# Performance work log

Measured on AMD Instinct MI355X. Metric: run time of the kernel, lower is better.

## Reference

```python
import jax, jax.numpy as jnp
import numpy as np
from jax.scipy.linalg import solve_triangular

NUM_EMBEDDINGS = 512
EMBEDDING_DIM = 64
SPARSITY = 5
COMMITMENT_COST = 0.25


def batch_omp(data, dictionary, max_nonzero):
    """Batch OMP. data: (M, B), dictionary: (M, N). Returns coeffs (N, B)."""
    M, B = data.shape
    Dt = dictionary.T                       # (N, M)
    G = Dt @ dictionary                     # (N, N) Gram matrix
    h_bar = (Dt @ data).T                   # (B, N)
    h = h_bar
    x = jnp.zeros_like(h_bar)               # (B, N)
    L = jnp.ones((B, 1, 1), data.dtype)     # growing Cholesky factor
    mask = jnp.zeros(h_bar.shape, dtype=bool)
    I = None                                # selected atom indices (B, k)
    bidx = jnp.arange(B)
    for k in range(1, max_nonzero + 1):     # small fixed unroll (5 iters)
        index = jnp.argmax(jnp.abs(h * (~mask)), axis=1)   # (B,)
        mask = mask.at[bidx, index].set(True)
        if k > 1:
            # G[I_b, index_b] for each batch element -> (B, k-1, 1)
            G_stack = G[I, index[:, None]][..., None]
            w = solve_triangular(L, G_stack, lower=True)   # (B, k-1, 1)
            wT = jnp.swapaxes(w, 1, 2)                     # (B, 1, k-1)
            w_corner = jnp.sqrt(jnp.clip(1.0 - jnp.sum(wT ** 2, axis=2, keepdims=True), 0.0))
            top = jnp.concatenate([L, jnp.zeros((B, k - 1, 1), L.dtype)], axis=2)
            bot = jnp.concatenate([wT, w_corner], axis=2)
            L = jnp.concatenate([top, bot], axis=1)        # (B, k, k)
            I = jnp.concatenate([I, index[:, None]], axis=1)
        else:
            I = index[:, None]
        h_stack = jnp.take_along_axis(h_bar, I, axis=1)[..., None]  # (B, k, 1)
        y = solve_triangular(L, h_stack, lower=True)
        x_stack = solve_triangular(jnp.swapaxes(L, 1, 2), y, lower=False)  # (B, k, 1)
        x = x.at[bidx[:, None], I].set(x_stack[..., 0])
        beta = jnp.einsum('bk,bkn->bn', x_stack[..., 0], G[I])  # (B, N)
        h = h_bar - beta
    return x.T                              # (N, B)


def setup_inputs() -> dict:
    key = jax.random.key(0)
    k1, k2 = jax.random.split(key)
    z_e = jax.random.normal(k1, (32, EMBEDDING_DIM, 32, 32), dtype=jnp.float32)
    D = jax.random.normal(k2, (EMBEDDING_DIM, NUM_EMBEDDINGS), dtype=jnp.float32)
    D = D / jnp.linalg.norm(D, axis=0)      # column-normalized atoms (as _normalize_dictionary)
    return {"z_e": z_e, "dictionary": D}


def reference(z_e, dictionary):
    # permute BCHW -> BHWC, then flat view to (embedding_dim, -1) row-major (as torch .view)
    z_perm = jnp.transpose(z_e, (0, 2, 3, 1))          # (B, H, W, C)
    input_shape = z_perm.shape
    ze_flat = z_perm.reshape(EMBEDDING_DIM, -1)        # (M, Btokens)
    coefficients = batch_omp(ze_flat, dictionary, SPARSITY)  # (N, Btokens)
    z_dl = (dictionary @ coefficients).reshape(input_shape)
    e_latent_loss = jnp.mean((jax.lax.stop_gradient(z_dl) - z_perm) ** 2)
    dl_latent_loss = jnp.mean((z_dl - jax.lax.stop_gradient(z_perm)) ** 2)
    loss = COMMITMENT_COST * e_latent_loss + dl_latent_loss
    z_out = z_perm + jax.lax.stop_gradient(z_dl - z_perm)   # straight-through
    return (jnp.transpose(z_out, (0, 3, 1, 2)), loss, coefficients)
```

## Files before the change

### kernel.cpp

```cpp
#include <hip/hip_runtime.h>

#define B_TOTAL 32768
#define NATOM   512
#define MDIM    64
#define KS      5

__global__ void k_perm(const float* __restrict__ ze, float* __restrict__ dT) {
    const int n   = blockIdx.x >> 4;
    const int hw0 = (blockIdx.x & 15) * 64;
    const int t   = threadIdx.x;
    __shared__ float lds[64][65];
#pragma unroll
    for (int r = 0; r < 16; ++r) {
        int id = r * 256 + t;
        int c = id >> 6, i = id & 63;
        lds[c][i] = ze[n * 65536 + c * 1024 + hw0 + i];
    }
    __syncthreads();
#pragma unroll
    for (int r = 0; r < 16; ++r) {
        int id = r * 256 + t;
        int c = id & 63, j = id >> 6;
        int hw = hw0 + j;
        int h = hw >> 5, w = hw & 31;
        int m = (n << 1) | (h >> 4);
        int b = ((h & 15) << 11) | (w << 6) | c;
        dT[m * 32768 + b] = lds[c][j];
    }
}

__global__ void k_gram(const float* __restrict__ D, float* __restrict__ G,
                       float* __restrict__ acc) {
    const int i = blockIdx.x;
    const int t = threadIdx.x;
    __shared__ float col[MDIM];
    if (t < MDIM) col[t] = D[t * NATOM + i];
    __syncthreads();
    for (int j = t; j < NATOM; j += 256) {
        float s = 0.f;
#pragma unroll
        for (int m = 0; m < MDIM; ++m) s = fmaf(col[m], D[m * NATOM + j], s);
        G[i * NATOM + j] = s;
    }
    if (i == 0 && t == 0) *acc = 0.f;
}

__launch_bounds__(256, 2)
__global__ void k_omp(const float* __restrict__ data, const float* __restrict__ D,
                      const float* __restrict__ G, int* __restrict__ idx_out,
                      float* __restrict__ val_out) {
    const int t    = threadIdx.x;
    const int lane = t & 63;
    const int wv   = t >> 6;
    const int b0   = blockIdx.x * 32;

    __shared__ __align__(16) float data_s[32][68];
    __shared__ __align__(16) float stage[4][2048];
    __shared__ int   idx_s[KS][32];
    __shared__ float val_s[KS][32];

#pragma unroll
    for (int r = 0; r < 8; ++r) {
        int id = r * 256 + t;
        int m = id >> 5, bb = id & 31;
        data_s[bb][m] = data[m * B_TOTAL + b0 + bb];
    }
    __syncthreads();

    const float4* __restrict__ D4 = (const float4*)D;
    const float4* __restrict__ G4 = (const float4*)G;

    float4 acc[8][2];
#pragma unroll
    for (int bb = 0; bb < 8; ++bb) {
        acc[bb][0] = make_float4(0.f, 0.f, 0.f, 0.f);
        acc[bb][1] = make_float4(0.f, 0.f, 0.f, 0.f);
    }
    const int bwbase = wv * 8;

#pragma unroll 4
    for (int c = 0; c < 16; ++c) {
        float4 df[4][2];
#pragma unroll
        for (int mm = 0; mm < 4; ++mm) {
            df[mm][0] = D4[(c * 4 + mm) * 128 + lane];
            df[mm][1] = D4[(c * 4 + mm) * 128 + 64 + lane];
        }
#pragma unroll
        for (int bb = 0; bb < 8; ++bb) {
            const float4 dv = *(const float4*)&data_s[bwbase + bb][c * 4];
            const float dm[4] = {dv.x, dv.y, dv.z, dv.w};
#pragma unroll
            for (int mm = 0; mm < 4; ++mm) {
                acc[bb][0].x = fmaf(df[mm][0].x, dm[mm], acc[bb][0].x);
                acc[bb][0].y = fmaf(df[mm][0].y, dm[mm], acc[bb][0].y);
                acc[bb][0].z = fmaf(df[mm][0].z, dm[mm], acc[bb][0].z);
                acc[bb][0].w = fmaf(df[mm][0].w, dm[mm], acc[bb][0].w);
                acc[bb][1].x = fmaf(df[mm][1].x, dm[mm], acc[bb][1].x);
                acc[bb][1].y = fmaf(df[mm][1].y, dm[mm], acc[bb][1].y);
                acc[bb][1].z = fmaf(df[mm][1].z, dm[mm], acc[bb][1].z);
                acc[bb][1].w = fmaf(df[mm][1].w, dm[mm], acc[bb][1].w);
            }
        }
    }

    const int g = lane >> 3;
    const int p = lane & 7;
    float hb[64];
#pragma unroll
    for (int r = 0; r < 2; ++r) {
        __syncthreads();
#pragma unroll
        for (int q2 = 0; q2 < 4; ++q2) {
            int bb = r * 4 + q2;
            *(float4*)&stage[wv][q2 * 512 + 4 * lane]       = acc[bb][0];
            *(float4*)&stage[wv][q2 * 512 + 256 + 4 * lane] = acc[bb][1];
        }
        __syncthreads();
        if ((g >> 2) == r) {
#pragma unroll
            for (int q = 0; q < 16; ++q) {
                const float4 v =
                    *(const float4*)&stage[wv][(g & 3) * 512 + 32 * q + 4 * p];
                hb[4 * q + 0] = v.x;
                hb[4 * q + 1] = v.y;
                hb[4 * q + 2] = v.z;
                hb[4 * q + 3] = v.w;
            }
        }
    }

    float key[64];
#pragma unroll
    for (int e = 0; e < 64; ++e) key[e] = fabsf(hb[e]);

    unsigned msk0 = 0u, msk1 = 0u;
    int   I[KS];
    float xs[KS];
    float gsel[KS];
    float Lm[15];

#pragma unroll
    for (int k = 0; k < KS; ++k) {
        float bv = key[0]; int be = 0; float bhb = hb[0];
#pragma unroll
        for (int e = 1; e < 64; ++e) {
            bool gt = key[e] > bv;
            bv  = gt ? key[e] : bv;
            be  = gt ? e      : be;
            bhb = gt ? hb[e]  : bhb;
        }
        int bn = 32 * (be >> 2) + 4 * p + (be & 3);
#pragma unroll
        for (int off = 1; off < 8; off <<= 1) {
            float ov  = __shfl_xor(bv, off);
            int   on  = __shfl_xor(bn, off);
            float ohb = __shfl_xor(bhb, off);
            bool take = (ov > bv) || (ov == bv && on < bn);
            bv = take ? ov : bv; bn = take ? on : bn; bhb = take ? ohb : bhb;
        }
        const int nsel = bn;
        I[k]    = nsel;
        gsel[k] = bhb;

        {
            int own  = (nsel >> 2) & 7;
            int esel = ((nsel >> 5) << 2) | (nsel & 3);
            if (p == own) {
                if (esel < 32) msk0 |= 1u << esel;
                else           msk1 |= 1u << (esel - 32);
            }
        }

        if (k > 0) {
            float gk[KS - 1], w[KS - 1];
#pragma unroll
            for (int ti = 0; ti < KS - 1; ++ti)
                if (ti < k) gk[ti] = G[I[ti] * NATOM + nsel];
#pragma unroll
            for (int r = 0; r < KS - 1; ++r) {
                if (r < k) {
                    float s = gk[r];
#pragma unroll
                    for (int cc = 0; cc < KS - 1; ++cc)
                        if (cc < r) s -= Lm[r * (r + 1) / 2 + cc] * w[cc];
                    w[r] = s / Lm[r * (r + 1) / 2 + r];
                }
            }
            float s2 = 0.f;
#pragma unroll
            for (int r = 0; r < KS - 1; ++r) if (r < k) s2 += w[r] * w[r];
            float wc = sqrtf(fmaxf(0.f, 1.f - s2));
#pragma unroll
            for (int cc = 0; cc < KS - 1; ++cc)
                if (cc < k) Lm[k * (k + 1) / 2 + cc] = w[cc];
            Lm[k * (k + 1) / 2 + k] = wc;
        } else {
            Lm[0] = 1.f;
        }

        float y[KS];
#pragma unroll
        for (int r = 0; r <= k; ++r) {
            float s = gsel[r];
#pragma unroll
            for (int cc = 0; cc < r; ++cc) s -= Lm[r * (r + 1) / 2 + cc] * y[cc];
            y[r] = s / Lm[r * (r + 1) / 2 + r];
        }
#pragma unroll
        for (int r = k; r >= 0; --r) {
            float s = y[r];
#pragma unroll
            for (int cc = r + 1; cc <= k; ++cc) s -= Lm[cc * (cc + 1) / 2 + r] * xs[cc];
            xs[r] = s / Lm[r * (r + 1) / 2 + r];
        }

        if (k < KS - 1) {
#pragma unroll
            for (int q = 0; q < 16; ++q) {
                float bx = 0.f, by = 0.f, bz = 0.f, bw = 0.f;
#pragma unroll
                for (int ti = 0; ti < KS - 1; ++ti) {
                    if (ti <= k) {
                        const float4 gc = G4[I[ti] * 128 + 8 * q + p];
                        bx = fmaf(xs[ti], gc.x, bx);
                        by = fmaf(xs[ti], gc.y, by);
                        bz = fmaf(xs[ti], gc.z, bz);
                        bw = fmaf(xs[ti], gc.w, bw);
                    }
                }
                {
                    float d0 = hb[4 * q + 0] - bx;
                    float d1 = hb[4 * q + 1] - by;
                    float d2 = hb[4 * q + 2] - bz;
                    float d3 = hb[4 * q + 3] - bw;
                    const int e0 = 4 * q;
                    bool m0 = (e0 + 0 < 32) ? ((msk0 >> (e0 + 0)) & 1u) : ((msk1 >> (e0 - 32)) & 1u);
                    bool m1 = (e0 + 1 < 32) ? ((msk0 >> (e0 + 1)) & 1u) : ((msk1 >> (e0 + 1 - 32)) & 1u);
                    bool m2 = (e0 + 2 < 32) ? ((msk0 >> (e0 + 2)) & 1u) : ((msk1 >> (e0 + 2 - 32)) & 1u);
                    bool m3 = (e0 + 3 < 32) ? ((msk0 >> (e0 + 3)) & 1u) : ((msk1 >> (e0 + 3 - 32)) & 1u);
                    key[e0 + 0] = m0 ? -1.f : fabsf(d0);
                    key[e0 + 1] = m1 ? -1.f : fabsf(d1);
                    key[e0 + 2] = m2 ? -1.f : fabsf(d2);
                    key[e0 + 3] = m3 ? -1.f : fabsf(d3);
                }
            }
        }
    }

    if (p == 0) {
#pragma unroll
        for (int k = 0; k < KS; ++k) {
            idx_s[k][wv * 8 + g] = I[k];
            val_s[k][wv * 8 + g] = xs[k];
        }
    }
    __syncthreads();
    if (t < KS * 32) {
        int k = t >> 5, bb = t & 31;
        idx_out[k * B_TOTAL + b0 + bb] = idx_s[k][bb];
        val_out[k * B_TOTAL + b0 + bb] = val_s[k][bb];
    }
}

__global__ void k_coeff(const int* __restrict__ idx, const float* __restrict__ val,
                        float* __restrict__ coeff) {
    const int bblk = blockIdx.x >> 3;
    const int jc   = blockIdx.x & 7;
    const int b    = bblk * 256 + threadIdx.x;
    int   I[KS]; float V[KS];
#pragma unroll
    for (int k = 0; k < KS; ++k) {
        I[k] = idx[k * B_TOTAL + b];
        V[k] = val[k * B_TOTAL + b];
    }
    const int j0 = jc * 64;
#pragma unroll 4
    for (int j = j0; j < j0 + 64; ++j) {
        float w = 0.f;
#pragma unroll
        for (int k = 0; k < KS; ++k) w = (I[k] == j) ? V[k] : w;
        coeff[j * B_TOTAL + b] = w;
    }
}

__global__ void k_recon(const float* __restrict__ dataT, const float* __restrict__ D,
                        const int* __restrict__ idx, const float* __restrict__ val,
                        float* __restrict__ zout, float* __restrict__ acc) {
    const int n   = blockIdx.x >> 4;
    const int hw0 = (blockIdx.x & 15) * 64;
    const int t   = threadIdx.x;
    __shared__ float lds[64][65];
    float sq = 0.f;
#pragma unroll
    for (int r = 0; r < 16; ++r) {
        int id = r * 256 + t;
        int c = id & 63, j = id >> 6;
        int f = n * 65536 + (hw0 + j) * 64 + c;
        int b = f & 32767;
        int m = f >> 15;
        float zdl = 0.f;
#pragma unroll
        for (int k = 0; k < KS; ++k) {
            int   a = idx[k * B_TOTAL + b];
            float v = val[k * B_TOTAL + b];
            zdl = fmaf(v, D[m * NATOM + a], zdl);
        }
        float zp   = dataT[f];
        float diff = zdl - zp;
        lds[c][j] = zp + diff;
        sq = fmaf(diff, diff, sq);
    }
    __syncthreads();
#pragma unroll
    for (int r = 0; r < 16; ++r) {
        int id = r * 256 + t;
        int cc = id >> 6, i = id & 63;
        zout[n * 65536 + cc * 1024 + hw0 + i] = lds[cc][i];
    }
#pragma unroll
    for (int off = 32; off > 0; off >>= 1) sq += __shfl_xor(sq, off);
    __shared__ float red[4];
    if ((t & 63) == 0) red[t >> 6] = sq;
    __syncthreads();
    if (t == 0) atomicAdd(acc, red[0] + red[1] + red[2] + red[3]);
}

__global__ void k_loss(const float* __restrict__ acc, float* __restrict__ out_loss) {
    if (threadIdx.x == 0 && blockIdx.x == 0)
        *out_loss = 1.25f * (*acc / 2097152.f);
}

extern "C" void kernel_launch(void* const* d_in, const int* in_sizes, int n_in,
                              void* d_out, int out_size, void* d_ws, size_t ws_size,
                              hipStream_t stream) {
    const float* ze = (const float*)d_in[0];
    const float* D  = (const float*)d_in[1];

    float* G     = (float*)d_ws;
    int*   idxp  = (int*)  ((char*)d_ws + (size_t)262144 * 4);
    float* valp  = (float*)((char*)d_ws + (size_t)(262144 + 163840) * 4);
    float* accp  = (float*)((char*)d_ws + (size_t)(262144 + 2 * 163840) * 4);
    float* dataT = (float*)((char*)d_ws + (size_t)(262144 + 2 * 163840 + 64) * 4);

    float* zout  = (float*)d_out;
    float* lossp = zout + 2097152;
    float* coeff = zout + 2097153;

    k_perm <<<512, 256, 0, stream>>>(ze, dataT);
    k_gram <<<512, 256, 0, stream>>>(D, G, accp);
    k_omp  <<<1024, 256, 0, stream>>>(dataT, D, G, idxp, valp);
    k_coeff<<<1024, 256, 0, stream>>>(idxp, valp, coeff);
    k_recon<<<512, 256, 0, stream>>>(dataT, D, idxp, valp, zout, accp);
    k_loss <<<1, 64, 0, stream>>>(accp, lossp);
}
```

Baseline: 186.9 us.

## Merge independent launches, keep residual h in registers with incremental update

Fuses the permute and Gram kernels into one launch, and the coefficient scatter and reconstruction kernels into another, cutting launch count from six to four. Inside the OMP kernel, the separate hb and key register arrays are replaced by a single residual array h. It is updated incrementally with the change in coefficients, and the argmax is split into four independent chains to shorten the dependency chain. The staging buffer is halved, and the selected h_bar value is rebuilt from the residual plus the Gram correction. This lowers register pressure and launch overhead, at the cost of possible small floating-point drift in the incremental residual.

```diff
diff --git a/kernel.cpp b/kernel.cpp
--- a/kernel.cpp
+++ b/kernel.cpp
@@ -5,44 +5,44 @@
 #define MDIM    64
 #define KS      5
 
-__global__ void k_perm(const float* __restrict__ ze, float* __restrict__ dT) {
-    const int n   = blockIdx.x >> 4;
-    const int hw0 = (blockIdx.x & 15) * 64;
-    const int t   = threadIdx.x;
+__global__ void k_prep(const float* __restrict__ ze, float* __restrict__ dT,
+                       const float* __restrict__ D, float* __restrict__ G,
+                       float* __restrict__ acc) {
     __shared__ float lds[64][65];
-#pragma unroll
-    for (int r = 0; r < 16; ++r) {
-        int id = r * 256 + t;
-        int c = id >> 6, i = id & 63;
-        lds[c][i] = ze[n * 65536 + c * 1024 + hw0 + i];
-    }
-    __syncthreads();
-#pragma unroll
-    for (int r = 0; r < 16; ++r) {
-        int id = r * 256 + t;
-        int c = id & 63, j = id >> 6;
-        int hw = hw0 + j;
-        int h = hw >> 5, w = hw & 31;
-        int m = (n << 1) | (h >> 4);
-        int b = ((h & 15) << 11) | (w << 6) | c;
-        dT[m * 32768 + b] = lds[c][j];
-    }
-}
-
-__global__ void k_gram(const float* __restrict__ D, float* __restrict__ G,
-                       float* __restrict__ acc) {
-    const int i = blockIdx.x;
     const int t = threadIdx.x;
-    __shared__ float col[MDIM];
-    if (t < MDIM) col[t] = D[t * NATOM + i];
-    __syncthreads();
-    for (int j = t; j < NATOM; j += 256) {
-        float s = 0.f;
-#pragma unroll
-        for (int m = 0; m < MDIM; ++m) s = fmaf(col[m], D[m * NATOM + j], s);
-        G[i * NATOM + j] = s;
-    }
-    if (i == 0 && t == 0) *acc = 0.f;
+    if (blockIdx.x < 512) {
+        const int n   = blockIdx.x >> 4;
+        const int hw0 = (blockIdx.x & 15) * 64;
+#pragma unroll
+        for (int r = 0; r < 16; ++r) {
+            int id = r * 256 + t;
+            int c = id >> 6, i = id & 63;
+            lds[c][i] = ze[n * 65536 + c * 1024 + hw0 + i];
+        }
+        __syncthreads();
+#pragma unroll
+        for (int r = 0; r < 16; ++r) {
+            int id = r * 256 + t;
+            int c = id & 63, j = id >> 6;
+            int hw = hw0 + j;
+            int h = hw >> 5, w = hw & 31;
+            int m = (n << 1) | (h >> 4);
+            int b = ((h & 15) << 11) | (w << 6) | c;
+            dT[m * 32768 + b] = lds[c][j];
+        }
+    } else {
+        const int i = blockIdx.x - 512;
+        float* col = &lds[0][0];
+        if (t < MDIM) col[t] = D[t * NATOM + i];
+        __syncthreads();
+        for (int j = t; j < NATOM; j += 256) {
+            float s = 0.f;
+#pragma unroll
+            for (int m = 0; m < MDIM; ++m) s = fmaf(col[m], D[m * NATOM + j], s);
+            G[i * NATOM + j] = s;
+        }
+        if (i == 0 && t == 0) *acc = 0.f;
+    }
 }
 
 __launch_bounds__(256, 2)
@@ -55,7 +55,7 @@
     const int b0   = blockIdx.x * 32;
 
     __shared__ __align__(16) float data_s[32][68];
-    __shared__ __align__(16) float stage[4][2048];
+    __shared__ __align__(16) float stage[4][1024];
     __shared__ int   idx_s[KS][32];
     __shared__ float val_s[KS][32];
 
@@ -106,33 +106,29 @@
 
     const int g = lane >> 3;
     const int p = lane & 7;
-    float hb[64];
-#pragma unroll
-    for (int r = 0; r < 2; ++r) {
-        __syncthreads();
-#pragma unroll
-        for (int q2 = 0; q2 < 4; ++q2) {
-            int bb = r * 4 + q2;
+    float h[64];
+#pragma unroll
+    for (int r = 0; r < 4; ++r) {
+        __syncthreads();
+#pragma unroll
+        for (int q2 = 0; q2 < 2; ++q2) {
+            int bb = r * 2 + q2;
             *(float4*)&stage[wv][q2 * 512 + 4 * lane]       = acc[bb][0];
             *(float4*)&stage[wv][q2 * 512 + 256 + 4 * lane] = acc[bb][1];
         }
         __syncthreads();
-        if ((g >> 2) == r) {
+        if ((g >> 1) == r) {
 #pragma unroll
             for (int q = 0; q < 16; ++q) {
                 const float4 v =
-                    *(const float4*)&stage[wv][(g & 3) * 512 + 32 * q + 4 * p];
-                hb[4 * q + 0] = v.x;
-                hb[4 * q + 1] = v.y;
-                hb[4 * q + 2] = v.z;
-                hb[4 * q + 3] = v.w;
-            }
-        }
-    }
-
-    float key[64];
-#pragma unroll
-    for (int e = 0; e < 64; ++e) key[e] = fabsf(hb[e]);
+                    *(const float4*)&stage[wv][(g & 1) * 512 + 32 * q + 4 * p];
+                h[4 * q + 0] = v.x;
+                h[4 * q + 1] = v.y;
+                h[4 * q + 2] = v.z;
+                h[4 * q + 3] = v.w;
+            }
+        }
+    }
 
     unsigned msk0 = 0u, msk1 = 0u;
     int   I[KS];
@@ -142,26 +138,38 @@
 
 #pragma unroll
     for (int k = 0; k < KS; ++k) {
-        float bv = key[0]; int be = 0; float bhb = hb[0];
-#pragma unroll
-        for (int e = 1; e < 64; ++e) {
-            bool gt = key[e] > bv;
-            bv  = gt ? key[e] : bv;
-            be  = gt ? e      : be;
-            bhb = gt ? hb[e]  : bhb;
+        float cv[4]; int ce[4]; float ch[4];
+#pragma unroll
+        for (int c4 = 0; c4 < 4; ++c4) {
+            cv[c4] = fabsf(h[16 * c4]); ce[c4] = 16 * c4; ch[c4] = h[16 * c4];
+#pragma unroll
+            for (int e = 16 * c4 + 1; e < 16 * c4 + 16; ++e) {
+                float a = fabsf(h[e]);
+                bool gt = a > cv[c4];
+                cv[c4] = gt ? a    : cv[c4];
+                ce[c4] = gt ? e    : ce[c4];
+                ch[c4] = gt ? h[e] : ch[c4];
+            }
+        }
+        float bv = cv[0]; int be = ce[0]; float bh = ch[0];
+#pragma unroll
+        for (int c4 = 1; c4 < 4; ++c4) {
+            bool gt = cv[c4] > bv;
+            bv = gt ? cv[c4] : bv;
+            be = gt ? ce[c4] : be;
+            bh = gt ? ch[c4] : bh;
         }
         int bn = 32 * (be >> 2) + 4 * p + (be & 3);
 #pragma unroll
         for (int off = 1; off < 8; off <<= 1) {
-            float ov  = __shfl_xor(bv, off);
-            int   on  = __shfl_xor(bn, off);
-            float ohb = __shfl_xor(bhb, off);
+            float ov = __shfl_xor(bv, off);
+            int   on = __shfl_xor(bn, off);
+            float oh = __shfl_xor(bh, off);
             bool take = (ov > bv) || (ov == bv && on < bn);
-            bv = take ? ov : bv; bn = take ? on : bn; bhb = take ? ohb : bhb;
+            bv = take ? ov : bv; bn = take ? on : bn; bh = take ? oh : bh;
         }
         const int nsel = bn;
-        I[k]    = nsel;
-        gsel[k] = bhb;
+        I[k] = nsel;
 
         {
             int own  = (nsel >> 2) & 7;
@@ -177,6 +185,11 @@
 #pragma unroll
             for (int ti = 0; ti < KS - 1; ++ti)
                 if (ti < k) gk[ti] = G[I[ti] * NATOM + nsel];
+            float hb_sel = bh;
+#pragma unroll
+            for (int ti = 0; ti < KS - 1; ++ti)
+                if (ti < k) hb_sel = fmaf(xs[ti], gk[ti], hb_sel);
+            gsel[k] = hb_sel;
 #pragma unroll
             for (int r = 0; r < KS - 1; ++r) {
                 if (r < k) {
@@ -196,6 +209,7 @@
                 if (cc < k) Lm[k * (k + 1) / 2 + cc] = w[cc];
             Lm[k * (k + 1) / 2 + k] = wc;
         } else {
+            gsel[0] = bh;
             Lm[0] = 1.f;
         }
 
@@ -207,6 +221,9 @@
             for (int cc = 0; cc < r; ++cc) s -= Lm[r * (r + 1) / 2 + cc] * y[cc];
             y[r] = s / Lm[r * (r + 1) / 2 + r];
         }
+        float dx[KS];
+#pragma unroll
+        for (int ti = 0; ti < KS; ++ti) dx[ti] = (ti < k) ? xs[ti] : 0.f;
 #pragma unroll
         for (int r = k; r >= 0; --r) {
             float s = y[r];
@@ -214,6 +231,8 @@
             for (int cc = r + 1; cc <= k; ++cc) s -= Lm[cc * (cc + 1) / 2 + r] * xs[cc];
             xs[r] = s / Lm[r * (r + 1) / 2 + r];
         }
+#pragma unroll
+        for (int ti = 0; ti < KS; ++ti) if (ti <= k) dx[ti] = xs[ti] - dx[ti];
 
         if (k < KS - 1) {
 #pragma unroll
@@ -223,26 +242,26 @@
                 for (int ti = 0; ti < KS - 1; ++ti) {
                     if (ti <= k) {
                         const float4 gc = G4[I[ti] * 128 + 8 * q + p];
-                        bx = fmaf(xs[ti], gc.x, bx);
-                        by = fmaf(xs[ti], gc.y, by);
-                        bz = fmaf(xs[ti], gc.z, bz);
-                        bw = fmaf(xs[ti], gc.w, bw);
+                        bx = fmaf(dx[ti], gc.x, bx);
+                        by = fmaf(dx[ti], gc.y, by);
+                        bz = fmaf(dx[ti], gc.z, bz);
+                        bw = fmaf(dx[ti], gc.w, bw);
                     }
                 }
                 {
-                    float d0 = hb[4 * q + 0] - bx;
-                    float d1 = hb[4 * q + 1] - by;
-                    float d2 = hb[4 * q + 2] - bz;
-                    float d3 = hb[4 * q + 3] - bw;
+                    float d0 = h[4 * q + 0] - bx;
+                    float d1 = h[4 * q + 1] - by;
+                    float d2 = h[4 * q + 2] - bz;
+                    float d3 = h[4 * q + 3] - bw;
                     const int e0 = 4 * q;
                     bool m0 = (e0 + 0 < 32) ? ((msk0 >> (e0 + 0)) & 1u) : ((msk1 >> (e0 - 32)) & 1u);
                     bool m1 = (e0 + 1 < 32) ? ((msk0 >> (e0 + 1)) & 1u) : ((msk1 >> (e0 + 1 - 32)) & 1u);
                     bool m2 = (e0 + 2 < 32) ? ((msk0 >> (e0 + 2)) & 1u) : ((msk1 >> (e0 + 2 - 32)) & 1u);
                     bool m3 = (e0 + 3 < 32) ? ((msk0 >> (e0 + 3)) & 1u) : ((msk1 >> (e0 + 3 - 32)) & 1u);
-                    key[e0 + 0] = m0 ? -1.f : fabsf(d0);
-                    key[e0 + 1] = m1 ? -1.f : fabsf(d1);
-                    key[e0 + 2] = m2 ? -1.f : fabsf(d2);
-                    key[e0 + 3] = m3 ? -1.f : fabsf(d3);
+                    h[e0 + 0] = m0 ? 0.f : d0;
+                    h[e0 + 1] = m1 ? 0.f : d1;
+                    h[e0 + 2] = m2 ? 0.f : d2;
+                    h[e0 + 3] = m3 ? 0.f : d3;
                 }
             }
         }
@@ -263,67 +282,68 @@
     }
 }
 
-__global__ void k_coeff(const int* __restrict__ idx, const float* __restrict__ val,
-                        float* __restrict__ coeff) {
-    const int bblk = blockIdx.x >> 3;
-    const int jc   = blockIdx.x & 7;
-    const int b    = bblk * 256 + threadIdx.x;
-    int   I[KS]; float V[KS];
-#pragma unroll
-    for (int k = 0; k < KS; ++k) {
-        I[k] = idx[k * B_TOTAL + b];
-        V[k] = val[k * B_TOTAL + b];
-    }
-    const int j0 = jc * 64;
+__global__ void k_post(const int* __restrict__ idx, const float* __restrict__ val,
+                       float* __restrict__ coeff, const float* __restrict__ dataT,
+                       const float* __restrict__ D, float* __restrict__ zout,
+                       float* __restrict__ acc) {
+    __shared__ float lds[64][65];
+    const int t = threadIdx.x;
+    if (blockIdx.x < 1024) {
+        const int bblk = blockIdx.x >> 3;
+        const int jc   = blockIdx.x & 7;
+        const int b    = bblk * 256 + t;
+        int   I[KS]; float V[KS];
+#pragma unroll
+        for (int k = 0; k < KS; ++k) {
+            I[k] = idx[k * B_TOTAL + b];
+            V[k] = val[k * B_TOTAL + b];
+        }
+        const int j0 = jc * 64;
 #pragma unroll 4
-    for (int j = j0; j < j0 + 64; ++j) {
-        float w = 0.f;
-#pragma unroll
-        for (int k = 0; k < KS; ++k) w = (I[k] == j) ? V[k] : w;
-        coeff[j * B_TOTAL + b] = w;
-    }
-}
-
-__global__ void k_recon(const float* __restrict__ dataT, const float* __restrict__ D,
-                        const int* __restrict__ idx, const float* __restrict__ val,
-                        float* __restrict__ zout, float* __restrict__ acc) {
-    const int n   = blockIdx.x >> 4;
-    const int hw0 = (blockIdx.x & 15) * 64;
-    const int t   = threadIdx.x;
-    __shared__ float lds[64][65];
-    float sq = 0.f;
-#pragma unroll
-    for (int r = 0; r < 16; ++r) {
-        int id = r * 256 + t;
-        int c = id & 63, j = id >> 6;
-        int f = n * 65536 + (hw0 + j) * 64 + c;
-        int b = f & 32767;
-        int m = f >> 15;
-        float zdl = 0.f;
-#pragma unroll
-        for (int k = 0; k < KS; ++k) {
-            int   a = idx[k * B_TOTAL + b];
-            float v = val[k * B_TOTAL + b];
-            zdl = fmaf(v, D[m * NATOM + a], zdl);
-        }
-        float zp   = dataT[f];
-        float diff = zdl - zp;
-        lds[c][j] = zp + diff;
-        sq = fmaf(diff, diff, sq);
-    }
-    __syncthreads();
-#pragma unroll
-    for (int r = 0; r < 16; ++r) {
-        int id = r * 256 + t;
-        int cc = id >> 6, i = id & 63;
-        zout[n * 65536 + cc * 1024 + hw0 + i] = lds[cc][i];
-    }
-#pragma unroll
-    for (int off = 32; off > 0; off >>= 1) sq += __shfl_xor(sq, off);
-    __shared__ float red[4];
-    if ((t & 63) == 0) red[t >> 6] = sq;
-    __syncthreads();
-    if (t == 0) atomicAdd(acc, red[0] + red[1] + red[2] + red[3]);
+        for (int j = j0; j < j0 + 64; ++j) {
+            float w = 0.f;
+#pragma unroll
+            for (int k = 0; k < KS; ++k) w = (I[k] == j) ? V[k] : w;
+            coeff[j * B_TOTAL + b] = w;
+        }
+    } else {
+        const int blk = blockIdx.x - 1024;
+        const int n   = blk >> 4;
+        const int hw0 = (blk & 15) * 64;
+        float sq = 0.f;
+#pragma unroll
+        for (int r = 0; r < 16; ++r) {
+            int id = r * 256 + t;
+            int c = id & 63, j = id >> 6;
+            int f = n * 65536 + (hw0 + j) * 64 + c;
+            int b = f & 32767;
+            int m = f >> 15;
+            float zdl = 0.f;
+#pragma unroll
+            for (int k = 0; k < KS; ++k) {
+                int   a = idx[k * B_TOTAL + b];
+                float v = val[k * B_TOTAL + b];
+                zdl = fmaf(v, D[m * NATOM + a], zdl);
+            }
+            float zp   = dataT[f];
+            float diff = zdl - zp;
+            lds[c][j] = zp + diff;
+            sq = fmaf(diff, diff, sq);
+        }
+        __syncthreads();
+#pragma unroll
+        for (int r = 0; r < 16; ++r) {
+            int id = r * 256 + t;
+            int cc = id >> 6, i = id & 63;
+            zout[n * 65536 + cc * 1024 + hw0 + i] = lds[cc][i];
+        }
+#pragma unroll
+        for (int off = 32; off > 0; off >>= 1) sq += __shfl_xor(sq, off);
+        __shared__ float red[4];
+        if ((t & 63) == 0) red[t >> 6] = sq;
+        __syncthreads();
+        if (t == 0) atomicAdd(acc, red[0] + red[1] + red[2] + red[3]);
+    }
 }
 
 __global__ void k_loss(const float* __restrict__ acc, float* __restrict__ out_loss) {
@@ -347,10 +367,8 @@
     float* lossp = zout + 2097152;
     float* coeff = zout + 2097153;
 
-    k_perm <<<512, 256, 0, stream>>>(ze, dataT);
-    k_gram <<<512, 256, 0, stream>>>(D, G, accp);
-    k_omp  <<<1024, 256, 0, stream>>>(dataT, D, G, idxp, valp);
-    k_coeff<<<1024, 256, 0, stream>>>(idxp, valp, coeff);
-    k_recon<<<512, 256, 0, stream>>>(dataT, D, idxp, valp, zout, accp);
-    k_loss <<<1, 64, 0, stream>>>(accp, lossp);
-}
+    k_prep<<<1024, 256, 0, stream>>>(ze, dataT, D, G, accp);
+    k_omp <<<1024, 256, 0, stream>>>(dataT, D, G, idxp, valp);
+    k_post<<<1536, 256, 0, stream>>>(idxp, valp, coeff, dataT, D, zout, accp);
+    k_loss<<<1, 64, 0, stream>>>(accp, lossp);
+}
```

Result: faster. 182.0 us (-2.6%).

## Merge independent kernels and shrink OMP blocks to single wavefronts

Applied to the files above, without the earlier changes.

Permute and Gram computation now share one launch, split by block index, and coefficient scatter and reconstruction share another, which cuts the kernel count from six to four. The OMP kernel drops from four wavefronts over 32 tokens to one wavefront over 8 tokens. This removes block-wide barriers and the LDS staging of results, and it lets the scheduler fit more small blocks per CU. In exchange, each block now loads the dictionary on its own, four times as often as before, and the larger number of small blocks adds scheduling overhead.

```diff
diff --git a/kernel.cpp b/kernel.cpp
--- a/kernel.cpp
+++ b/kernel.cpp
@@ -5,64 +5,60 @@
 #define MDIM    64
 #define KS      5
 
-__global__ void k_perm(const float* __restrict__ ze, float* __restrict__ dT) {
-    const int n   = blockIdx.x >> 4;
-    const int hw0 = (blockIdx.x & 15) * 64;
-    const int t   = threadIdx.x;
+__global__ void k_prep(const float* __restrict__ ze, float* __restrict__ dT,
+                       const float* __restrict__ D, float* __restrict__ G,
+                       float* __restrict__ acc) {
     __shared__ float lds[64][65];
-#pragma unroll
-    for (int r = 0; r < 16; ++r) {
-        int id = r * 256 + t;
-        int c = id >> 6, i = id & 63;
-        lds[c][i] = ze[n * 65536 + c * 1024 + hw0 + i];
-    }
-    __syncthreads();
-#pragma unroll
-    for (int r = 0; r < 16; ++r) {
-        int id = r * 256 + t;
-        int c = id & 63, j = id >> 6;
-        int hw = hw0 + j;
-        int h = hw >> 5, w = hw & 31;
-        int m = (n << 1) | (h >> 4);
-        int b = ((h & 15) << 11) | (w << 6) | c;
-        dT[m * 32768 + b] = lds[c][j];
-    }
-}
-
-__global__ void k_gram(const float* __restrict__ D, float* __restrict__ G,
-                       float* __restrict__ acc) {
-    const int i = blockIdx.x;
     const int t = threadIdx.x;
-    __shared__ float col[MDIM];
-    if (t < MDIM) col[t] = D[t * NATOM + i];
-    __syncthreads();
-    for (int j = t; j < NATOM; j += 256) {
-        float s = 0.f;
-#pragma unroll
-        for (int m = 0; m < MDIM; ++m) s = fmaf(col[m], D[m * NATOM + j], s);
-        G[i * NATOM + j] = s;
-    }
-    if (i == 0 && t == 0) *acc = 0.f;
-}
-
-__launch_bounds__(256, 2)
+    if (blockIdx.x < 512) {
+        const int n   = blockIdx.x >> 4;
+        const int hw0 = (blockIdx.x & 15) * 64;
+#pragma unroll
+        for (int r = 0; r < 16; ++r) {
+            int id = r * 256 + t;
+            int c = id >> 6, i = id & 63;
+            lds[c][i] = ze[n * 65536 + c * 1024 + hw0 + i];
+        }
+        __syncthreads();
+#pragma unroll
+        for (int r = 0; r < 16; ++r) {
+            int id = r * 256 + t;
+            int c = id & 63, j = id >> 6;
+            int hw = hw0 + j;
+            int h = hw >> 5, w = hw & 31;
+            int m = (n << 1) | (h >> 4);
+            int b = ((h & 15) << 11) | (w << 6) | c;
+            dT[m * 32768 + b] = lds[c][j];
+        }
+    } else {
+        const int i = blockIdx.x - 512;
+        float* col = &lds[0][0];
+        if (t < MDIM) col[t] = D[t * NATOM + i];
+        __syncthreads();
+        for (int j = t; j < NATOM; j += 256) {
+            float s = 0.f;
+#pragma unroll
+            for (int m = 0; m < MDIM; ++m) s = fmaf(col[m], D[m * NATOM + j], s);
+            G[i * NATOM + j] = s;
+        }
+        if (i == 0 && t == 0) *acc = 0.f;
+    }
+}
+
+__launch_bounds__(64, 4)
 __global__ void k_omp(const float* __restrict__ data, const float* __restrict__ D,
                       const float* __restrict__ G, int* __restrict__ idx_out,
                       float* __restrict__ val_out) {
-    const int t    = threadIdx.x;
-    const int lane = t & 63;
-    const int wv   = t >> 6;
-    const int b0   = blockIdx.x * 32;
-
-    __shared__ __align__(16) float data_s[32][68];
-    __shared__ __align__(16) float stage[4][2048];
-    __shared__ int   idx_s[KS][32];
-    __shared__ float val_s[KS][32];
+    const int lane = threadIdx.x;
+    const int b0   = blockIdx.x * 8;
+
+    __shared__ __align__(16) float data_s[8][68];
+    __shared__ __align__(16) float stage[2048];
 
 #pragma unroll
     for (int r = 0; r < 8; ++r) {
-        int id = r * 256 + t;
-        int m = id >> 5, bb = id & 31;
+        int id = r * 64 + lane;
+        int m = id >> 3, bb = id & 7;
         data_s[bb][m] = data[m * B_TOTAL + b0 + bb];
     }
     __syncthreads();
@@ -76,7 +72,6 @@
         acc[bb][0] = make_float4(0.f, 0.f, 0.f, 0.f);
         acc[bb][1] = make_float4(0.f, 0.f, 0.f, 0.f);
     }
-    const int bwbase = wv * 8;
 
 #pragma unroll 4
     for (int c = 0; c < 16; ++c) {
@@ -88,7 +83,7 @@
         }
 #pragma unroll
         for (int bb = 0; bb < 8; ++bb) {
-            const float4 dv = *(const float4*)&data_s[bwbase + bb][c * 4];
+            const float4 dv = *(const float4*)&data_s[bb][c * 4];
             const float dm[4] = {dv.x, dv.y, dv.z, dv.w};
 #pragma unroll
             for (int mm = 0; mm < 4; ++mm) {
@@ -113,15 +108,15 @@
 #pragma unroll
         for (int q2 = 0; q2 < 4; ++q2) {
             int bb = r * 4 + q2;
-            *(float4*)&stage[wv][q2 * 512 + 4 * lane]       = acc[bb][0];
-            *(float4*)&stage[wv][q2 * 512 + 256 + 4 * lane] = acc[bb][1];
+            *(float4*)&stage[q2 * 512 + 4 * lane]       = acc[bb][0];
+            *(float4*)&stage[q2 * 512 + 256 + 4 * lane] = acc[bb][1];
         }
         __syncthreads();
         if ((g >> 2) == r) {
 #pragma unroll
             for (int q = 0; q < 16; ++q) {
                 const float4 v =
-                    *(const float4*)&stage[wv][(g & 3) * 512 + 32 * q + 4 * p];
+                    *(const float4*)&stage[(g & 3) * 512 + 32 * q + 4 * p];
                 hb[4 * q + 0] = v.x;
                 hb[4 * q + 1] = v.y;
                 hb[4 * q + 2] = v.z;
@@ -251,79 +246,74 @@
     if (p == 0) {
 #pragma unroll
         for (int k = 0; k < KS; ++k) {
-            idx_s[k][wv * 8 + g] = I[k];
-            val_s[k][wv * 8 + g] = xs[k];
-        }
-    }
-    __syncthreads();
-    if (t < KS * 32) {
-        int k = t >> 5, bb = t & 31;
-        idx_out[k * B_TOTAL + b0 + bb] = idx_s[k][bb];
-        val_out[k * B_TOTAL + b0 + bb] = val_s[k][bb];
-    }
-}
-
-__global__ void k_coeff(const int* __restrict__ idx, const float* __restrict__ val,
-                        float* __restrict__ coeff) {
-    const int bblk = blockIdx.x >> 3;
-    const int jc   = blockIdx.x & 7;
-    const int b    = bblk * 256 + threadIdx.x;
-    int   I[KS]; float V[KS];
-#pragma unroll
-    for (int k = 0; k < KS; ++k) {
-        I[k] = idx[k * B_TOTAL + b];
-        V[k] = val[k * B_TOTAL + b];
-    }
-    const int j0 = jc * 64;
+            idx_out[k * B_TOTAL + b0 + g] = I[k];
+            val_out[k * B_TOTAL + b0 + g] = xs[k];
+        }
+    }
+}
+
+__global__ void k_post(const int* __restrict__ idx, const float* __restrict__ val,
+                       float* __restrict__ coeff, const float* __restrict__ dataT,
+                       const float* __restrict__ D, float* __restrict__ zout,
+                       float* __restrict__ acc) {
+    __shared__ float lds[64][65];
+    const int t = threadIdx.x;
+    if (blockIdx.x < 1024) {
+        const int bblk = blockIdx.x >> 3;
+        const int jc   = blockIdx.x & 7;
+        const int b    = bblk * 256 + t;
+        int   I[KS]; float V[KS];
+#pragma unroll
+        for (int k = 0; k < KS; ++k) {
+            I[k] = idx[k * B_TOTAL + b];
+            V[k] = val[k * B_TOTAL + b];
+        }
+        const int j0 = jc * 64;
 #pragma unroll 4
-    for (int j = j0; j < j0 + 64; ++j) {
-        float w = 0.f;
-#pragma unroll
-        for (int k = 0; k < KS; ++k) w = (I[k] == j) ? V[k] : w;
-        coeff[j * B_TOTAL + b] = w;
-    }
-}
-
-__global__ void k_recon(const float* __restrict__ dataT, const float* __restrict__ D,
-                        const int* __restrict__ idx, const float* __restrict__ val,
-                        float* __restrict__ zout, float* __restrict__ acc) {
-    const int n   = blockIdx.x >> 4;
-    const int hw0 = (blockIdx.x & 15) * 64;
-    const int t   = threadIdx.x;
-    __shared__ float lds[64][65];
-    float sq = 0.f;
-#pragma unroll
-    for (int r = 0; r < 16; ++r) {
-        int id = r * 256 + t;
-        int c = id & 63, j = id >> 6;
-        int f = n * 65536 + (hw0 + j) * 64 + c;
-        int b = f & 32767;
-        int m = f >> 15;
-        float zdl = 0.f;
-#pragma unroll
-        for (int k = 0; k < KS; ++k) {
-            int   a = idx[k * B_TOTAL + b];
-            float v = val[k * B_TOTAL + b];
-            zdl = fmaf(v, D[m * NATOM + a], zdl);
-        }
-        float zp   = dataT[f];
-        float diff = zdl - zp;
-        lds[c][j] = zp + diff;
-        sq = fmaf(diff, diff, sq);
-    }
-    __syncthreads();
-#pragma unroll
-    for (int r = 0; r < 16; ++r) {
-        int id = r * 256 + t;
-        int cc = id >> 6, i = id & 63;
-        zout[n * 65536 + cc * 1024 + hw0 + i] = lds[cc][i];
-    }
-#pragma unroll
-    for (int off = 32; off > 0; off >>= 1) sq += __shfl_xor(sq, off);
-    __shared__ float red[4];
-    if ((t & 63) == 0) red[t >> 6] = sq;
-    __syncthreads();
-    if (t == 0) atomicAdd(acc, red[0] + red[1] + red[2] + red[3]);
+        for (int j = j0; j < j0 + 64; ++j) {
+            float w = 0.f;
+#pragma unroll
+            for (int k = 0; k < KS; ++k) w = (I[k] == j) ? V[k] : w;
+            coeff[j * B_TOTAL + b] = w;
+        }
+    } else {
+        const int blk = blockIdx.x - 1024;
+        const int n   = blk >> 4;
+        const int hw0 = (blk & 15) * 64;
+        float sq = 0.f;
+#pragma unroll
+        for (int r = 0; r < 16; ++r) {
+            int id = r * 256 + t;
+            int c = id & 63, j = id >> 6;
+            int f = n * 65536 + (hw0 + j) * 64 + c;
+            int b = f & 32767;
+            int m = f >> 15;
+            float zdl = 0.f;
+#pragma unroll
+            for (int k = 0; k < KS; ++k) {
+                int   a = idx[k * B_TOTAL + b];
+                float v = val[k * B_TOTAL + b];
+                zdl = fmaf(v, D[m * NATOM + a], zdl);
+            }
+            float zp   = dataT[f];
+            float diff = zdl - zp;
+            lds[c][j] = zp + diff;
+            sq = fmaf(diff, diff, sq);
+        }
+        __syncthreads();
+#pragma unroll
+        for (int r = 0; r < 16; ++r) {
+            int id = r * 256 + t;
+            int cc = id >> 6, i = id & 63;
+            zout[n * 65536 + cc * 1024 + hw0 + i] = lds[cc][i];
+        }
+#pragma unroll
+        for (int off = 32; off > 0; off >>= 1) sq += __shfl_xor(sq, off);
+        __shared__ float red[4];
+        if ((t & 63) == 0) red[t >> 6] = sq;
+        __syncthreads();
+        if (t == 0) atomicAdd(acc, red[0] + red[1] + red[2] + red[3]);
+    }
 }
 
 __global__ void k_loss(const float* __restrict__ acc, float* __restrict__ out_loss) {
@@ -347,10 +337,8 @@
     float* lossp = zout + 2097152;
     float* coeff = zout + 2097153;
 
-    k_perm <<<512, 256, 0, stream>>>(ze, dataT);
-    k_gram <<<512, 256, 0, stream>>>(D, G, accp);
-    k_omp  <<<1024, 256, 0, stream>>>(dataT, D, G, idxp, valp);
-    k_coeff<<<1024, 256, 0, stream>>>(idxp, valp, coeff);
-    k_recon<<<512, 256, 0, stream>>>(dataT, D, idxp, valp, zout, accp);
-    k_loss <<<1, 64, 0, stream>>>(accp, lossp);
-}
+    k_prep<<<1024, 256, 0, stream>>>(ze, dataT, D, G, accp);
+    k_omp <<<4096,  64, 0, stream>>>(dataT, D, G, idxp, valp);
+    k_post<<<1536, 256, 0, stream>>>(idxp, valp, coeff, dataT, D, zout, accp);
+    k_loss<<<1, 64, 0, stream>>>(accp, lossp);
+}
```

Result: slower. 390.6 us (+109.0%).
